# Optimization experiments

Measured on AMD Instinct MI355X. Metric: run time of the kernel, lower is better.

Reference implementation:

```python
import jax, jax.numpy as jnp
import numpy as np

B, L, D = 1, 256, 256
H, DK, R = 8, 32, 2
EPS = 1e-6


def _proj_ode(x, t, W, b, r):
    """Stand-in for ODELinear/InterpLinear: linear projection of x broadcast
    over a second time index with r exponential time-decay coefficients.
    x: [B,L,D], t: [B,L] -> [B,L,L,r,D_out]"""
    base = x @ W.T + b                                  # [B,L,Do]
    dt = jnp.abs(t[:, :, None] - t[:, None, :])         # [B,L,L]
    steps = jnp.linspace(0.0, 1.0, r, dtype=x.dtype)    # [r]
    coef = jnp.exp(-dt[:, :, :, None] * steps)          # [B,L,L,r]
    return coef[..., None] * base[:, None, :, None, :]  # [B,L,L,r,Do]


def _layer_norm(x, g, b):
    mu = x.mean(-1, keepdims=True)
    var = ((x - mu) ** 2).mean(-1, keepdims=True)
    return (x - mu) * jax.lax.rsqrt(var + EPS) * g + b


def setup_inputs() -> dict:
    key = jax.random.key(0)
    ks = jax.random.split(key, 12)
    s = 1.0 / np.sqrt(D)
    return {
        "q": jax.random.normal(ks[0], (B, L, D), jnp.float32),
        "k": jax.random.normal(ks[1], (B, L, D), jnp.float32),
        "v": jax.random.normal(ks[2], (B, L, D), jnp.float32),
        "t": jax.random.uniform(ks[3], (B, L), jnp.float32),
        "Wq": jax.random.normal(ks[4], (D, D), jnp.float32) * s,
        "bq": jnp.zeros((D,), jnp.float32),
        "Wk": jax.random.normal(ks[5], (D, D), jnp.float32) * s,
        "bk": jnp.zeros((D,), jnp.float32),
        "Wv": jax.random.normal(ks[6], (D, D), jnp.float32) * s,
        "bv": jnp.zeros((D,), jnp.float32),
        "fc_w": jax.random.normal(ks[7], (D, D), jnp.float32) * s,
        "fc_b": jnp.zeros((D,), jnp.float32),
        "ln_g": jnp.ones((D,), jnp.float32),
        "ln_b": jnp.zeros((D,), jnp.float32),
    }


def reference(q, k, v, t, Wq, bq, Wk, bk, Wv, bv, fc_w, fc_b, ln_g, ln_b):
    temp = DK ** 0.5
    residual = q
    qn = _layer_norm(q, ln_g, ln_b)  # normalize_before=True (only q)

    # [B,L,L,R,D] -> [B,L,L,R,H,DK] -> [B,H,L,L,R,DK]
    def to6(x):
        return x.reshape(B, L, L, R, H, DK).transpose(0, 4, 1, 2, 3, 5)

    qp = to6(_proj_ode(qn, t, Wq, bq, R))
    kp = to6(_proj_ode(k, t, Wk, bk, R))
    vp = to6(_proj_ode(v, t, Wv, bv, R))

    # attn = (q/temp * k).sum(-1).sum(-1): multiply-reduce over (R, DK), no matmul
    attn = jnp.einsum('bhijrd,bhijrd->bhij', qp, kp) / temp
    attn = jax.nn.softmax(attn, axis=-1)  # dropout=0 (eval)

    vs = vp.sum(axis=4)                                   # reduce R: [B,H,L,L,DK]
    out = jnp.einsum('bhij,bhijd->bhid', attn, vs)        # reduce second L
    out = out.transpose(0, 2, 1, 3).reshape(B, L, H * DK)
    out = out @ fc_w.T + fc_b
    out = out + residual
    return (out, attn)
```

## Files before the change

### kernel.cpp

```cpp
#include <hip/hip_runtime.h>
#include <math.h>


#define INV_TEMP 0.17677669529663687f

__global__ __launch_bounds__(256) void k_ln(const float* __restrict__ q,
                                            const float* __restrict__ g,
                                            const float* __restrict__ b,
                                            float* __restrict__ qn) {
  const int row  = (blockIdx.x << 2) + (threadIdx.x >> 6);
  const int lane = threadIdx.x & 63;
  float4 x = ((const float4*)(q + (row << 8)))[lane];
  float s = x.x + x.y + x.z + x.w;
#pragma unroll
  for (int off = 32; off; off >>= 1) s += __shfl_xor(s, off);
  const float mu = s * 0.00390625f;
  const float d0 = x.x - mu, d1 = x.y - mu, d2 = x.z - mu, d3 = x.w - mu;
  float var = d0 * d0 + d1 * d1 + d2 * d2 + d3 * d3;
#pragma unroll
  for (int off = 32; off; off >>= 1) var += __shfl_xor(var, off);
  const float rs = rsqrtf(var * 0.00390625f + 1e-6f);
  const float4 gv = ((const float4*)g)[lane];
  const float4 bv = ((const float4*)b)[lane];
  float4 y;
  y.x = d0 * rs * gv.x + bv.x;
  y.y = d1 * rs * gv.y + bv.y;
  y.z = d2 * rs * gv.z + bv.z;
  y.w = d3 * rs * gv.w + bv.w;
  ((float4*)(qn + (row << 8)))[lane] = y;
}

__device__ __forceinline__ void gemm_body(const float* __restrict__ X,
                                          const float* __restrict__ W,
                                          const float* __restrict__ bias,
                                          const float* __restrict__ res,
                                          float* __restrict__ out) {
  __shared__ float As[32][34];
  __shared__ float Bs[32][34];
  const int t  = threadIdx.x;
  const int j0 = blockIdx.y << 5, o0 = blockIdx.x << 5;
  const int tx = t & 15, ty = t >> 4;
  const int lr = t >> 3, lc = (t & 7) << 2;
  float acc00 = 0.f, acc01 = 0.f, acc10 = 0.f, acc11 = 0.f;
  for (int k0 = 0; k0 < 256; k0 += 32) {
    const float4 a = *(const float4*)(X + ((j0 + lr) << 8) + k0 + lc);
    const float4 w = *(const float4*)(W + ((o0 + lr) << 8) + k0 + lc);
    if (k0) __syncthreads();
    As[lc + 0][lr] = a.x; As[lc + 1][lr] = a.y;
    As[lc + 2][lr] = a.z; As[lc + 3][lr] = a.w;
    Bs[lc + 0][lr] = w.x; Bs[lc + 1][lr] = w.y;
    Bs[lc + 2][lr] = w.z; Bs[lc + 3][lr] = w.w;
    __syncthreads();
#pragma unroll
    for (int kk = 0; kk < 32; ++kk) {
      const float2 av = *(const float2*)&As[kk][ty << 1];
      const float2 bv = *(const float2*)&Bs[kk][tx << 1];
      acc00 = fmaf(av.x, bv.x, acc00);
      acc01 = fmaf(av.x, bv.y, acc01);
      acc10 = fmaf(av.y, bv.x, acc10);
      acc11 = fmaf(av.y, bv.y, acc11);
    }
  }
  const int j = j0 + (ty << 1), o = o0 + (tx << 1);
  const float b0 = bias[o], b1 = bias[o + 1];
  float r00 = 0.f, r01 = 0.f, r10 = 0.f, r11 = 0.f;
  if (res) {
    r00 = res[(j << 8) + o];       r01 = res[(j << 8) + o + 1];
    r10 = res[((j + 1) << 8) + o]; r11 = res[((j + 1) << 8) + o + 1];
  }
  out[(j << 8) + o]           = acc00 + b0 + r00;
  out[(j << 8) + o + 1]       = acc01 + b1 + r01;
  out[((j + 1) << 8) + o]     = acc10 + b0 + r10;
  out[((j + 1) << 8) + o + 1] = acc11 + b1 + r11;
}

__global__ __launch_bounds__(256) void k_gemm3(
    const float* __restrict__ qn, const float* __restrict__ kin,
    const float* __restrict__ vin, const float* __restrict__ Wq,
    const float* __restrict__ bq, const float* __restrict__ Wk,
    const float* __restrict__ bk, const float* __restrict__ Wv,
    const float* __restrict__ bv, float* __restrict__ baseQ,
    float* __restrict__ baseK, float* __restrict__ baseV) {
  if (blockIdx.z == 0)       gemm_body(qn,  Wq, bq, nullptr, baseQ);
  else if (blockIdx.z == 1)  gemm_body(kin, Wk, bk, nullptr, baseK);
  else                       gemm_body(vin, Wv, bv, nullptr, baseV);
}

__global__ __launch_bounds__(256) void k_fc(const float* __restrict__ ctxf,
                                            const float* __restrict__ fc_w,
                                            const float* __restrict__ fc_b,
                                            const float* __restrict__ q,
                                            float* __restrict__ out) {
  gemm_body(ctxf, fc_w, fc_b, q, out);
}

__global__ __launch_bounds__(512) void k_attn(const float* __restrict__ baseQ,
                                              const float* __restrict__ baseK,
                                              const float* __restrict__ baseV,
                                              const float* __restrict__ tt,
                                              float* __restrict__ attn_out,
                                              float* __restrict__ ctxf) {
  const int h  = blockIdx.y;
  const int i0 = blockIdx.x << 3;
  __shared__ float s_lds[256];
  __shared__ float P[8][256];
  const int t = threadIdx.x;
  if (t < 256) {
    const float4* qr = (const float4*)(baseQ + (t << 8) + (h << 5));
    const float4* kr = (const float4*)(baseK + (t << 8) + (h << 5));
    float acc = 0.f;
#pragma unroll
    for (int u = 0; u < 8; ++u) {
      const float4 a = qr[u], b = kr[u];
      acc += a.x * b.x + a.y * b.y + a.z * b.z + a.w * b.w;
    }
    s_lds[t] = acc * INV_TEMP;
  }
  __syncthreads();

  const int w = t >> 6, lane = t & 63;
  const int i = i0 + w;
  const float ti = tt[i];
  const float4 tj = ((const float4*)tt)[lane];
  const float4 sv = ((const float4*)s_lds)[lane];
  const float e0 = __expf(-fabsf(ti - tj.x));
  const float e1 = __expf(-fabsf(ti - tj.y));
  const float e2 = __expf(-fabsf(ti - tj.z));
  const float e3 = __expf(-fabsf(ti - tj.w));
  const float sc0 = (1.f + e0 * e0) * sv.x;
  const float sc1 = (1.f + e1 * e1) * sv.y;
  const float sc2 = (1.f + e2 * e2) * sv.z;
  const float sc3 = (1.f + e3 * e3) * sv.w;
  float m = fmaxf(fmaxf(sc0, sc1), fmaxf(sc2, sc3));
#pragma unroll
  for (int off = 32; off; off >>= 1) m = fmaxf(m, __shfl_xor(m, off));
  float p0 = __expf(sc0 - m), p1 = __expf(sc1 - m);
  float p2 = __expf(sc2 - m), p3 = __expf(sc3 - m);
  float s = p0 + p1 + p2 + p3;
#pragma unroll
  for (int off = 32; off; off >>= 1) s += __shfl_xor(s, off);
  const float rinv = 1.f / s;
  p0 *= rinv; p1 *= rinv; p2 *= rinv; p3 *= rinv;
  const float4 av = make_float4(p0, p1, p2, p3);
  ((float4*)(attn_out + (((h << 8) + i) << 8)))[lane] = av;
  const float4 pv = make_float4(p0 * (1.f + e0), p1 * (1.f + e1),
                                p2 * (1.f + e2), p3 * (1.f + e3));
  ((float4*)P[w])[lane] = pv;

  const int dk = lane & 31, half = lane >> 5;
  const float* Pr = P[w] + (half << 7);
  const float* Vp = baseV + (h << 5) + dk + ((half << 7) << 8);
  float a0 = 0.f, a1 = 0.f, a2 = 0.f, a3 = 0.f;
#pragma unroll 4
  for (int jj = 0; jj < 128; jj += 4) {
    a0 = fmaf(Pr[jj + 0], Vp[(jj + 0) << 8], a0);
    a1 = fmaf(Pr[jj + 1], Vp[(jj + 1) << 8], a1);
    a2 = fmaf(Pr[jj + 2], Vp[(jj + 2) << 8], a2);
    a3 = fmaf(Pr[jj + 3], Vp[(jj + 3) << 8], a3);
  }
  float acc = (a0 + a1) + (a2 + a3);
  acc += __shfl_xor(acc, 32);
  if (half == 0) ctxf[(i << 8) + (h << 5) + dk] = acc;
}

extern "C" void kernel_launch(void* const* d_in, const int* in_sizes, int n_in,
                              void* d_out, int out_size, void* d_ws,
                              size_t ws_size, hipStream_t stream) {
  const float* q    = (const float*)d_in[0];
  const float* k    = (const float*)d_in[1];
  const float* v    = (const float*)d_in[2];
  const float* tt   = (const float*)d_in[3];
  const float* Wq   = (const float*)d_in[4];
  const float* bq   = (const float*)d_in[5];
  const float* Wk   = (const float*)d_in[6];
  const float* bk   = (const float*)d_in[7];
  const float* Wv   = (const float*)d_in[8];
  const float* bv   = (const float*)d_in[9];
  const float* fc_w = (const float*)d_in[10];
  const float* fc_b = (const float*)d_in[11];
  const float* ln_g = (const float*)d_in[12];
  const float* ln_b = (const float*)d_in[13];

  float* out  = (float*)d_out;
  float* attn = out + 65536;

  float* ws    = (float*)d_ws;
  float* qn    = ws;
  float* baseQ = ws + 65536;
  float* baseK = ws + 131072;
  float* baseV = ws + 196608;
  float* ctxf  = ws + 262144;

  hipLaunchKernelGGL(k_ln, dim3(64), dim3(256), 0, stream, q, ln_g, ln_b, qn);
  hipLaunchKernelGGL(k_gemm3, dim3(8, 8, 3), dim3(256), 0, stream, qn, k, v,
                     Wq, bq, Wk, bk, Wv, bv, baseQ, baseK, baseV);
  hipLaunchKernelGGL(k_attn, dim3(32, 8), dim3(512), 0, stream, baseQ, baseK,
                     baseV, tt, attn, ctxf);
  hipLaunchKernelGGL(k_fc, dim3(8, 8), dim3(256), 0, stream, ctxf, fc_w, fc_b,
                     q, out);
}
```

Measured before the change: 105.6 us.

## Fuse LayerNorm into projection GEMM, load full K panel, transpose Q/K outputs

Removes the separate LayerNorm kernel by computing row mean and variance inside the Q projection GEMM, which now loads the whole 256-wide K dimension into LDS at once instead of looping over 32-wide tiles. Q and K projections are written transposed so the attention score pass reads coalesced columns per thread. This drops one kernel launch and the qn round trip through memory, and cuts per-tile synchronisation. In exchange LDS use per block grows substantially, which may lower occupancy, and variance is computed as E[x^2]-mu^2, which is less numerically stable.

```diff
diff --git a/kernel.cpp b/kernel.cpp
--- a/kernel.cpp
+++ b/kernel.cpp
@@ -4,116 +4,126 @@
 
 #define INV_TEMP 0.17677669529663687f
 
-__global__ __launch_bounds__(256) void k_ln(const float* __restrict__ q,
-                                            const float* __restrict__ g,
-                                            const float* __restrict__ b,
-                                            float* __restrict__ qn) {
-  const int row  = (blockIdx.x << 2) + (threadIdx.x >> 6);
-  const int lane = threadIdx.x & 63;
-  float4 x = ((const float4*)(q + (row << 8)))[lane];
-  float s = x.x + x.y + x.z + x.w;
-#pragma unroll
-  for (int off = 32; off; off >>= 1) s += __shfl_xor(s, off);
-  const float mu = s * 0.00390625f;
-  const float d0 = x.x - mu, d1 = x.y - mu, d2 = x.z - mu, d3 = x.w - mu;
-  float var = d0 * d0 + d1 * d1 + d2 * d2 + d3 * d3;
-#pragma unroll
-  for (int off = 32; off; off >>= 1) var += __shfl_xor(var, off);
-  const float rs = rsqrtf(var * 0.00390625f + 1e-6f);
-  const float4 gv = ((const float4*)g)[lane];
-  const float4 bv = ((const float4*)b)[lane];
-  float4 y;
-  y.x = d0 * rs * gv.x + bv.x;
-  y.y = d1 * rs * gv.y + bv.y;
-  y.z = d2 * rs * gv.z + bv.z;
-  y.w = d3 * rs * gv.w + bv.w;
-  ((float4*)(qn + (row << 8)))[lane] = y;
-}
-
-__device__ __forceinline__ void gemm_body(const float* __restrict__ X,
-                                          const float* __restrict__ W,
-                                          const float* __restrict__ bias,
-                                          const float* __restrict__ res,
-                                          float* __restrict__ out) {
-  __shared__ float As[32][34];
-  __shared__ float Bs[32][34];
-  const int t  = threadIdx.x;
+__device__ __forceinline__ void gemm_panel(
+    const float* __restrict__ X, const float* __restrict__ W,
+    const float* __restrict__ bias, const float* __restrict__ res,
+    const float* __restrict__ ln_g, const float* __restrict__ ln_b,
+    float* __restrict__ out, const int mode) {
+  __shared__ float As[256][33];
+  __shared__ float Bs[256][33];
+  const int t = threadIdx.x;
   const int j0 = blockIdx.y << 5, o0 = blockIdx.x << 5;
+  const int lr = t >> 3;
+  const int cg = (t & 7) << 2;
+  float4 xa[8], wb[8];
+#pragma unroll
+  for (int u = 0; u < 8; ++u) {
+    xa[u] = *(const float4*)(X + ((j0 + lr) << 8) + (u << 5) + cg);
+    wb[u] = *(const float4*)(W + ((o0 + lr) << 8) + (u << 5) + cg);
+  }
+  if (mode == 0) {
+    float s = 0.f, s2 = 0.f;
+#pragma unroll
+    for (int u = 0; u < 8; ++u) {
+      s  += xa[u].x + xa[u].y + xa[u].z + xa[u].w;
+      s2 += xa[u].x * xa[u].x + xa[u].y * xa[u].y +
+            xa[u].z * xa[u].z + xa[u].w * xa[u].w;
+    }
+#pragma unroll
+    for (int off = 1; off < 8; off <<= 1) {
+      s  += __shfl_xor(s, off);
+      s2 += __shfl_xor(s2, off);
+    }
+    const float mu = s * 0.00390625f;
+    const float rs = rsqrtf(s2 * 0.00390625f - mu * mu + 1e-6f);
+#pragma unroll
+    for (int u = 0; u < 8; ++u) {
+      const float4 gv = *(const float4*)(ln_g + (u << 5) + cg);
+      const float4 bv = *(const float4*)(ln_b + (u << 5) + cg);
+      xa[u].x = (xa[u].x - mu) * rs * gv.x + bv.x;
+      xa[u].y = (xa[u].y - mu) * rs * gv.y + bv.y;
+      xa[u].z = (xa[u].z - mu) * rs * gv.z + bv.z;
+      xa[u].w = (xa[u].w - mu) * rs * gv.w + bv.w;
+    }
+  }
+#pragma unroll
+  for (int u = 0; u < 8; ++u) {
+    const int c = (u << 5) + cg;
+    As[c + 0][lr] = xa[u].x; As[c + 1][lr] = xa[u].y;
+    As[c + 2][lr] = xa[u].z; As[c + 3][lr] = xa[u].w;
+    Bs[c + 0][lr] = wb[u].x; Bs[c + 1][lr] = wb[u].y;
+    Bs[c + 2][lr] = wb[u].z; Bs[c + 3][lr] = wb[u].w;
+  }
+  __syncthreads();
   const int tx = t & 15, ty = t >> 4;
-  const int lr = t >> 3, lc = (t & 7) << 2;
   float acc00 = 0.f, acc01 = 0.f, acc10 = 0.f, acc11 = 0.f;
-  for (int k0 = 0; k0 < 256; k0 += 32) {
-    const float4 a = *(const float4*)(X + ((j0 + lr) << 8) + k0 + lc);
-    const float4 w = *(const float4*)(W + ((o0 + lr) << 8) + k0 + lc);
-    if (k0) __syncthreads();
-    As[lc + 0][lr] = a.x; As[lc + 1][lr] = a.y;
-    As[lc + 2][lr] = a.z; As[lc + 3][lr] = a.w;
-    Bs[lc + 0][lr] = w.x; Bs[lc + 1][lr] = w.y;
-    Bs[lc + 2][lr] = w.z; Bs[lc + 3][lr] = w.w;
-    __syncthreads();
-#pragma unroll
-    for (int kk = 0; kk < 32; ++kk) {
-      const float2 av = *(const float2*)&As[kk][ty << 1];
-      const float2 bv = *(const float2*)&Bs[kk][tx << 1];
-      acc00 = fmaf(av.x, bv.x, acc00);
-      acc01 = fmaf(av.x, bv.y, acc01);
-      acc10 = fmaf(av.y, bv.x, acc10);
-      acc11 = fmaf(av.y, bv.y, acc11);
-    }
+#pragma unroll 16
+  for (int kk = 0; kk < 256; ++kk) {
+    const float2 av = *(const float2*)&As[kk][ty << 1];
+    const float2 bv = *(const float2*)&Bs[kk][tx << 1];
+    acc00 = fmaf(av.x, bv.x, acc00);
+    acc01 = fmaf(av.x, bv.y, acc01);
+    acc10 = fmaf(av.y, bv.x, acc10);
+    acc11 = fmaf(av.y, bv.y, acc11);
   }
   const int j = j0 + (ty << 1), o = o0 + (tx << 1);
   const float b0 = bias[o], b1 = bias[o + 1];
-  float r00 = 0.f, r01 = 0.f, r10 = 0.f, r11 = 0.f;
-  if (res) {
-    r00 = res[(j << 8) + o];       r01 = res[(j << 8) + o + 1];
-    r10 = res[((j + 1) << 8) + o]; r11 = res[((j + 1) << 8) + o + 1];
-  }
-  out[(j << 8) + o]           = acc00 + b0 + r00;
-  out[(j << 8) + o + 1]       = acc01 + b1 + r01;
-  out[((j + 1) << 8) + o]     = acc10 + b0 + r10;
-  out[((j + 1) << 8) + o + 1] = acc11 + b1 + r11;
-}
-
-__global__ __launch_bounds__(256) void k_gemm3(
-    const float* __restrict__ qn, const float* __restrict__ kin,
+  acc00 += b0; acc01 += b1; acc10 += b0; acc11 += b1;
+  if (mode <= 1) {
+    *(float2*)(out + (o << 8) + j)       = make_float2(acc00, acc10);
+    *(float2*)(out + ((o + 1) << 8) + j) = make_float2(acc01, acc11);
+  } else {
+    float2 r0 = make_float2(0.f, 0.f), r1 = make_float2(0.f, 0.f);
+    if (mode == 3) {
+      r0 = *(const float2*)(res + (j << 8) + o);
+      r1 = *(const float2*)(res + ((j + 1) << 8) + o);
+    }
+    *(float2*)(out + (j << 8) + o) = make_float2(acc00 + r0.x, acc01 + r0.y);
+    *(float2*)(out + ((j + 1) << 8) + o) =
+        make_float2(acc10 + r1.x, acc11 + r1.y);
+  }
+}
+
+__global__ __launch_bounds__(256) void mha_proj_gemm3(
+    const float* __restrict__ q, const float* __restrict__ kin,
     const float* __restrict__ vin, const float* __restrict__ Wq,
     const float* __restrict__ bq, const float* __restrict__ Wk,
     const float* __restrict__ bk, const float* __restrict__ Wv,
-    const float* __restrict__ bv, float* __restrict__ baseQ,
-    float* __restrict__ baseK, float* __restrict__ baseV) {
-  if (blockIdx.z == 0)       gemm_body(qn,  Wq, bq, nullptr, baseQ);
-  else if (blockIdx.z == 1)  gemm_body(kin, Wk, bk, nullptr, baseK);
-  else                       gemm_body(vin, Wv, bv, nullptr, baseV);
-}
-
-__global__ __launch_bounds__(256) void k_fc(const float* __restrict__ ctxf,
-                                            const float* __restrict__ fc_w,
-                                            const float* __restrict__ fc_b,
-                                            const float* __restrict__ q,
-                                            float* __restrict__ out) {
-  gemm_body(ctxf, fc_w, fc_b, q, out);
-}
-
-__global__ __launch_bounds__(512) void k_attn(const float* __restrict__ baseQ,
-                                              const float* __restrict__ baseK,
-                                              const float* __restrict__ baseV,
-                                              const float* __restrict__ tt,
-                                              float* __restrict__ attn_out,
-                                              float* __restrict__ ctxf) {
-  const int h  = blockIdx.y;
+    const float* __restrict__ bv, const float* __restrict__ ln_g,
+    const float* __restrict__ ln_b, float* __restrict__ baseQT,
+    float* __restrict__ baseKT, float* __restrict__ baseV) {
+  const int z = blockIdx.z;
+  if (z == 0)
+    gemm_panel(q, Wq, bq, nullptr, ln_g, ln_b, baseQT, 0);
+  else if (z == 1)
+    gemm_panel(kin, Wk, bk, nullptr, nullptr, nullptr, baseKT, 1);
+  else
+    gemm_panel(vin, Wv, bv, nullptr, nullptr, nullptr, baseV, 2);
+}
+
+__global__ __launch_bounds__(256) void mha_fc_gemm(
+    const float* __restrict__ ctxf, const float* __restrict__ fc_w,
+    const float* __restrict__ fc_b, const float* __restrict__ q,
+    float* __restrict__ out) {
+  gemm_panel(ctxf, fc_w, fc_b, q, nullptr, nullptr, out, 3);
+}
+
+__global__ __launch_bounds__(512) void mha_attn_fused(
+    const float* __restrict__ baseQT, const float* __restrict__ baseKT,
+    const float* __restrict__ baseV, const float* __restrict__ tt,
+    float* __restrict__ attn_out, float* __restrict__ ctxf) {
+  const int h = blockIdx.y;
   const int i0 = blockIdx.x << 3;
+  const int t = threadIdx.x;
   __shared__ float s_lds[256];
   __shared__ float P[8][256];
-  const int t = threadIdx.x;
   if (t < 256) {
-    const float4* qr = (const float4*)(baseQ + (t << 8) + (h << 5));
-    const float4* kr = (const float4*)(baseK + (t << 8) + (h << 5));
+    const float* qc = baseQT + (h << 13) + t;
+    const float* kc = baseKT + (h << 13) + t;
     float acc = 0.f;
 #pragma unroll
-    for (int u = 0; u < 8; ++u) {
-      const float4 a = qr[u], b = kr[u];
-      acc += a.x * b.x + a.y * b.y + a.z * b.z + a.w * b.w;
-    }
+    for (int dk = 0; dk < 32; ++dk)
+      acc = fmaf(qc[dk << 8], kc[dk << 8], acc);
     s_lds[t] = acc * INV_TEMP;
   }
   __syncthreads();
@@ -141,15 +151,14 @@
   for (int off = 32; off; off >>= 1) s += __shfl_xor(s, off);
   const float rinv = 1.f / s;
   p0 *= rinv; p1 *= rinv; p2 *= rinv; p3 *= rinv;
-  const float4 av = make_float4(p0, p1, p2, p3);
-  ((float4*)(attn_out + (((h << 8) + i) << 8)))[lane] = av;
-  const float4 pv = make_float4(p0 * (1.f + e0), p1 * (1.f + e1),
-                                p2 * (1.f + e2), p3 * (1.f + e3));
-  ((float4*)P[w])[lane] = pv;
+  ((float4*)(attn_out + (((h << 8) + i) << 8)))[lane] =
+      make_float4(p0, p1, p2, p3);
+  ((float4*)P[w])[lane] = make_float4(p0 * (1.f + e0), p1 * (1.f + e1),
+                                      p2 * (1.f + e2), p3 * (1.f + e3));
 
   const int dk = lane & 31, half = lane >> 5;
   const float* Pr = P[w] + (half << 7);
-  const float* Vp = baseV + (h << 5) + dk + ((half << 7) << 8);
+  const float* Vp = baseV + (h << 5) + dk + (half << 15);
   float a0 = 0.f, a1 = 0.f, a2 = 0.f, a3 = 0.f;
 #pragma unroll 4
   for (int jj = 0; jj < 128; jj += 4) {
@@ -167,8 +176,8 @@
                               void* d_out, int out_size, void* d_ws,
                               size_t ws_size, hipStream_t stream) {
   const float* q    = (const float*)d_in[0];
-  const float* k    = (const float*)d_in[1];
-  const float* v    = (const float*)d_in[2];
+  const float* kin  = (const float*)d_in[1];
+  const float* vin  = (const float*)d_in[2];
   const float* tt   = (const float*)d_in[3];
   const float* Wq   = (const float*)d_in[4];
   const float* bq   = (const float*)d_in[5];
@@ -184,18 +193,17 @@
   float* out  = (float*)d_out;
   float* attn = out + 65536;
 
-  float* ws    = (float*)d_ws;
-  float* qn    = ws;
-  float* baseQ = ws + 65536;
-  float* baseK = ws + 131072;
-  float* baseV = ws + 196608;
-  float* ctxf  = ws + 262144;
-
-  hipLaunchKernelGGL(k_ln, dim3(64), dim3(256), 0, stream, q, ln_g, ln_b, qn);
-  hipLaunchKernelGGL(k_gemm3, dim3(8, 8, 3), dim3(256), 0, stream, qn, k, v,
-                     Wq, bq, Wk, bk, Wv, bv, baseQ, baseK, baseV);
-  hipLaunchKernelGGL(k_attn, dim3(32, 8), dim3(512), 0, stream, baseQ, baseK,
-                     baseV, tt, attn, ctxf);
-  hipLaunchKernelGGL(k_fc, dim3(8, 8), dim3(256), 0, stream, ctxf, fc_w, fc_b,
-                     q, out);
-}
+  float* ws     = (float*)d_ws;
+  float* baseQT = ws;
+  float* baseKT = ws + 65536;
+  float* baseV  = ws + 131072;
+  float* ctxf   = ws + 196608;
+
+  hipLaunchKernelGGL(mha_proj_gemm3, dim3(8, 8, 3), dim3(256), 0, stream, q,
+                     kin, vin, Wq, bq, Wk, bk, Wv, bv, ln_g, ln_b, baseQT,
+                     baseKT, baseV);
+  hipLaunchKernelGGL(mha_attn_fused, dim3(32, 8), dim3(512), 0, stream,
+                     baseQT, baseKT, baseV, tt, attn, ctxf);
+  hipLaunchKernelGGL(mha_fc_gemm, dim3(8, 8), dim3(256), 0, stream, ctxf,
+                     fc_w, fc_b, q, out);
+}
```

Result: faster. 100.4 us (-4.9%).
